# Kernel tuning notes

Hardware: AMD Instinct MI355X
Metric: run time of the kernel (lower is better)

Reference implementation:

```python
import jax, jax.numpy as jnp
import numpy as np

B, H, KVH, D = 64, 32, 8, 128     # batch, q heads, kv heads, head dim
BS, MB = 16, 128                  # paged-cache block size, max blocks per seq
NB = B * MB                       # total cache blocks (8192)
L = MB * BS                       # max kv length per sequence (2048)
SCALE = 0.08838834764831845       # 1/sqrt(head_dim)


def setup_inputs() -> dict:
    key = jax.random.key(0)
    ks = jax.random.split(key, 6)
    q = jax.random.normal(ks[0], (B, H * D), jnp.float32)
    k = jax.random.normal(ks[1], (B, KVH * D), jnp.float32)
    v = jax.random.normal(ks[2], (B, KVH * D), jnp.float32)
    k_cache = jax.random.normal(ks[3], (NB, BS, KVH, D), jnp.float32)
    v_cache = jax.random.normal(ks[4], (NB, BS, KVH, D), jnp.float32)
    # each sequence owns MB disjoint contiguous blocks
    block_tables = jnp.arange(B * MB, dtype=jnp.int32).reshape(B, MB)
    context_lens = jax.random.randint(ks[5], (B,), 0, L - 1, dtype=jnp.int32)
    return dict(q=q, k=k, v=v, k_cache=k_cache, v_cache=v_cache,
                block_tables=block_tables, context_lens=context_lens)


def reference(q, k, v, k_cache, v_cache, block_tables, context_lens):
    G = H // KVH  # GQA group size
    qh = q.reshape(B, KVH, G, D)
    kh = k.reshape(B, KVH, D)
    vh = v.reshape(B, KVH, D)
    # store new token's KV at its paged slot (position = context_len)
    slots = block_tables[jnp.arange(B), context_lens // BS] * BS + context_lens % BS
    kc = k_cache.reshape(NB * BS, KVH, D).at[slots].set(kh)
    vc = v_cache.reshape(NB * BS, KVH, D).at[slots].set(vh)
    # gather paged KV per sequence via block tables -> [B, L, KVH, D]
    keys = kc.reshape(NB, BS, KVH, D)[block_tables].reshape(B, L, KVH, D)
    vals = vc.reshape(NB, BS, KVH, D)[block_tables].reshape(B, L, KVH, D)
    # GQA attention: each kv head serves G query heads
    scores = jnp.einsum('bkgd,blkd->bkgl', qh, keys) * SCALE
    valid = jnp.arange(L)[None, :] <= context_lens[:, None]  # [B, L], inclusive of new token
    scores = jnp.where(valid[:, None, None, :], scores, jnp.float32(-jnp.inf))
    w = jax.nn.softmax(scores, axis=-1)
    out = jnp.einsum('bkgl,blkd->bkgd', w, vals)
    return out.reshape(B, H * D)
```

## Files before the change

### kernel.cpp

```cpp
#include <hip/hip_runtime.h>

#define BATCH 64
#define NHEADS 32
#define KVH 8
#define HDIM 128
#define GQA 4
#define BLKSZ 16
#define MAXBLK 128
#define MAXLEN 2048
#define SCALE 0.08838834764831845f

#define CHUNK 64
#define NPART (MAXLEN / CHUNK)
#define GSTRIDE 144
#define SLOT_BYTES 4096u
#define WS_FLOATS ((size_t)BATCH * NPART * KVH * GQA * GSTRIDE)

typedef unsigned int uint;
typedef float f32x4 __attribute__((ext_vector_type(4)));

struct KVBuf { float4 k0, k1, v0, v1; };

template<int CTRL>
__device__ __forceinline__ float dppAdd(float x) {
    int y = __builtin_amdgcn_update_dpp(0, __float_as_int(x), CTRL, 0xf, 0xf, false);
    return x + __int_as_float(y);
}

__device__ __forceinline__ float halfSum(float v, bool upper) {
    v = dppAdd<0x111>(v);
    v = dppAdd<0x112>(v);
    v = dppAdd<0x114>(v);
    v = dppAdd<0x118>(v);
    v = dppAdd<0x142>(v);
    const float lo = __int_as_float(__builtin_amdgcn_readlane(__float_as_int(v), 31));
    const float hi = __int_as_float(__builtin_amdgcn_readlane(__float_as_int(v), 63));
    return upper ? hi : lo;
}

__global__ __launch_bounds__(256, 4) void pa_partial(
    const float* __restrict__ q,
    const float* __restrict__ knew,
    const float* __restrict__ vnew,
    const float* __restrict__ k_cache,
    const float* __restrict__ v_cache,
    const int*   __restrict__ block_tables,
    const int*   __restrict__ context_lens,
    float* __restrict__ ws)
{
    const int bid  = blockIdx.x;
    const int part = bid & (NPART - 1);
    const int b    = bid >> 5;

    const int cl = context_lens[b];
    const int n  = cl + 1;
    const int p0 = part * CHUNK;
    if (p0 >= n) return;
    const int pend = min(p0 + CHUNK, n);

    const int tid  = threadIdx.x;
    const int kvh  = tid >> 5;
    const int lane = tid & 31;
    const bool upperHalf = (tid & 32) != 0;
    const uint laneByte = ((uint)kvh << 9) + ((uint)lane << 4);

    float4 qf[GQA];
    #pragma unroll
    for (int g = 0; g < GQA; ++g) {
        float4 t = *reinterpret_cast<const float4*>(
            &q[(size_t)b * (NHEADS * HDIM) + (size_t)(kvh * GQA + g) * HDIM + lane * 4]);
        t.x *= SCALE; t.y *= SCALE; t.z *= SCALE; t.w *= SCALE;
        qf[g] = t;
    }

    float  s[GQA];
    float4 acc[GQA];
    #pragma unroll
    for (int g = 0; g < GQA; ++g) {
        s[g] = 0.f;
        acc[g] = make_float4(0.f, 0.f, 0.f, 0.f);
    }

    const char* kc8 = reinterpret_cast<const char*>(k_cache);
    const char* vc8 = reinterpret_cast<const char*>(v_cache);

    if (p0 + CHUNK <= cl) {
        int blkv[4];
        #pragma unroll
        for (int c = 0; c < 4; ++c)
            blkv[c] = block_tables[b * MAXBLK + (p0 >> 4) + c];

        KVBuf bufA, bufB;

#define ISSUE(P, i)                                                              \
        {                                                                        \
            const uint u0 = ((uint)blkv[(2*(i)) >> 4] * BLKSZ + ((2*(i)) & 15)) * SLOT_BYTES + laneByte; \
            const uint u1 = ((uint)blkv[(2*(i)+1) >> 4] * BLKSZ + ((2*(i)+1) & 15)) * SLOT_BYTES + laneByte; \
            buf##P.k0 = *reinterpret_cast<const float4*>(kc8 + u0);              \
            buf##P.k1 = *reinterpret_cast<const float4*>(kc8 + u1);              \
            buf##P.v0 = *reinterpret_cast<const float4*>(vc8 + u0);              \
            buf##P.v1 = *reinterpret_cast<const float4*>(vc8 + u1);              \
        }

#define CONSUME(P)                                                               \
        {                                                                        \
            float sc0[GQA], sc1[GQA];                                            \
            _Pragma("unroll")                                                    \
            for (int g = 0; g < GQA; ++g) {                                      \
                sc0[g] = buf##P.k0.x * qf[g].x + buf##P.k0.y * qf[g].y           \
                       + buf##P.k0.z * qf[g].z + buf##P.k0.w * qf[g].w;          \
                sc1[g] = buf##P.k1.x * qf[g].x + buf##P.k1.y * qf[g].y           \
                       + buf##P.k1.z * qf[g].z + buf##P.k1.w * qf[g].w;          \
            }                                                                    \
            _Pragma("unroll")                                                    \
            for (int g = 0; g < GQA; ++g) {                                      \
                sc0[g] = halfSum(sc0[g], upperHalf);                             \
                sc1[g] = halfSum(sc1[g], upperHalf);                             \
            }                                                                    \
            _Pragma("unroll")                                                    \
            for (int g = 0; g < GQA; ++g) {                                      \
                const float e0 = __expf(sc0[g]);                                 \
                const float e1 = __expf(sc1[g]);                                 \
                s[g] += e0 + e1;                                                 \
                acc[g].x += e0 * buf##P.v0.x + e1 * buf##P.v1.x;                 \
                acc[g].y += e0 * buf##P.v0.y + e1 * buf##P.v1.y;                 \
                acc[g].z += e0 * buf##P.v0.z + e1 * buf##P.v1.z;                 \
                acc[g].w += e0 * buf##P.v0.w + e1 * buf##P.v1.w;                 \
            }                                                                    \
        }

        ISSUE(A, 0);
        #pragma unroll
        for (int i = 0; i < 31; ++i) {
            if (i & 1) { ISSUE(A, i + 1); CONSUME(B); }
            else       { ISSUE(B, i + 1); CONSUME(A); }
        }
        CONSUME(B);
#undef ISSUE
#undef CONSUME
    } else {
        const int* bt = &block_tables[b * MAXBLK];
        const float* knrow = &knew[((size_t)b * KVH + kvh) * HDIM + lane * 4];
        const float* vnrow = &vnew[((size_t)b * KVH + kvh) * HDIM + lane * 4];

        for (int t0 = p0; t0 < pend; t0 += 4) {
            bool valid[4];
            const float* kp[4];
            const float* vp[4];
            #pragma unroll
            for (int j = 0; j < 4; ++j) {
                const int l = t0 + j;
                valid[j] = (l < pend);
                if (!valid[j] || l == cl) {
                    kp[j] = knrow; vp[j] = vnrow;
                } else {
                    const int blk = bt[l >> 4];
                    const uint u  = ((uint)blk * BLKSZ + (l & 15)) * SLOT_BYTES + laneByte;
                    kp[j] = reinterpret_cast<const float*>(kc8 + u);
                    vp[j] = reinterpret_cast<const float*>(vc8 + u);
                }
            }

            float4 kf[4], vf[4];
            #pragma unroll
            for (int j = 0; j < 4; ++j) kf[j] = *reinterpret_cast<const float4*>(kp[j]);
            #pragma unroll
            for (int j = 0; j < 4; ++j) vf[j] = *reinterpret_cast<const float4*>(vp[j]);

            float sc[4][GQA];
            #pragma unroll
            for (int j = 0; j < 4; ++j)
                #pragma unroll
                for (int g = 0; g < GQA; ++g)
                    sc[j][g] = kf[j].x * qf[g].x + kf[j].y * qf[g].y
                             + kf[j].z * qf[g].z + kf[j].w * qf[g].w;

            #pragma unroll
            for (int off = 16; off > 0; off >>= 1)
                #pragma unroll
                for (int j = 0; j < 4; ++j)
                    #pragma unroll
                    for (int g = 0; g < GQA; ++g)
                        sc[j][g] += __shfl_xor(sc[j][g], off, 32);

            #pragma unroll
            for (int g = 0; g < GQA; ++g) {
                float p[4];
                #pragma unroll
                for (int j = 0; j < 4; ++j)
                    p[j] = valid[j] ? __expf(sc[j][g]) : 0.f;
                s[g] += (p[0] + p[1]) + (p[2] + p[3]);
                acc[g].x += p[0] * vf[0].x + p[1] * vf[1].x + p[2] * vf[2].x + p[3] * vf[3].x;
                acc[g].y += p[0] * vf[0].y + p[1] * vf[1].y + p[2] * vf[2].y + p[3] * vf[3].y;
                acc[g].z += p[0] * vf[0].z + p[1] * vf[1].z + p[2] * vf[2].z + p[3] * vf[3].z;
                acc[g].w += p[0] * vf[0].w + p[1] * vf[1].w + p[2] * vf[2].w + p[3] * vf[3].w;
            }
        }
    }

    float* rec = ws + ((size_t)(bid * KVH + kvh) * GQA) * GSTRIDE;
    #pragma unroll
    for (int g = 0; g < GQA; ++g)
        *reinterpret_cast<float4*>(rec + (size_t)g * GSTRIDE + lane * 4) = acc[g];
    if (lane == 0) {
        #pragma unroll
        for (int g = 0; g < GQA; ++g) rec[(size_t)g * GSTRIDE + 128] = s[g];
    }
}

__global__ __launch_bounds__(128) void pa_reduce(
    const float* __restrict__ ws,
    const int*   __restrict__ context_lens,
    float* __restrict__ out)
{
    const int bh   = blockIdx.x;
    const int b    = bh >> 3;
    const int kvh  = bh & 7;
    const int t    = threadIdx.x;
    const int g    = t >> 5;
    const int lane = t & 31;

    const int n    = context_lens[b] + 1;
    const int pcnt = (n + CHUNK - 1) / CHUNK;

    const float* base = ws + ((size_t)((b * NPART) * KVH + kvh) * GQA + g) * GSTRIDE;
    const size_t pstride = (size_t)KVH * GQA * GSTRIDE;

    f32x4 O0 = {0,0,0,0}, O1 = {0,0,0,0}, O2 = {0,0,0,0}, O3 = {0,0,0,0};
    float S0 = 0.f, S1 = 0.f, S2 = 0.f, S3 = 0.f;
    int p = 0;
    for (; p + 4 <= pcnt; p += 4) {
        const float* r0 = base + (p + 0) * pstride;
        const float* r1 = base + (p + 1) * pstride;
        const float* r2 = base + (p + 2) * pstride;
        const float* r3 = base + (p + 3) * pstride;
        O0 += *reinterpret_cast<const f32x4*>(r0 + lane * 4);
        O1 += *reinterpret_cast<const f32x4*>(r1 + lane * 4);
        O2 += *reinterpret_cast<const f32x4*>(r2 + lane * 4);
        O3 += *reinterpret_cast<const f32x4*>(r3 + lane * 4);
        S0 += r0[128]; S1 += r1[128]; S2 += r2[128]; S3 += r3[128];
    }
    for (; p < pcnt; ++p) {
        const float* r = base + p * pstride;
        O0 += *reinterpret_cast<const f32x4*>(r + lane * 4);
        S0 += r[128];
    }
    const f32x4 O = (O0 + O1) + (O2 + O3);
    const float S = (S0 + S1) + (S2 + S3);
    const float inv = 1.0f / S;

    float* op = &out[(size_t)b * (NHEADS * HDIM) + (size_t)(kvh * GQA + g) * HDIM + lane * 4];
    *reinterpret_cast<f32x4*>(op) = O * inv;
}

__global__ __launch_bounds__(256) void paged_attn_decode(
    const float* __restrict__ q,
    const float* __restrict__ knew,
    const float* __restrict__ vnew,
    const float* __restrict__ k_cache,
    const float* __restrict__ v_cache,
    const int*   __restrict__ block_tables,
    const int*   __restrict__ context_lens,
    float* __restrict__ out)
{
    const int bh   = blockIdx.x;
    const int b    = bh / KVH;
    const int kvh  = bh % KVH;
    const int tid  = threadIdx.x;
    const int hw   = tid >> 5;
    const int lane = tid & 31;

    const int cl = context_lens[b];
    const int n  = cl + 1;

    float4 qf[GQA];
    #pragma unroll
    for (int g = 0; g < GQA; ++g) {
        float4 t = *reinterpret_cast<const float4*>(
            &q[(size_t)b * (NHEADS * HDIM) + (size_t)(kvh * GQA + g) * HDIM + lane * 4]);
        t.x *= SCALE; t.y *= SCALE; t.z *= SCALE; t.w *= SCALE;
        qf[g] = t;
    }

    float  s[GQA];
    float4 acc[GQA];
    #pragma unroll
    for (int g = 0; g < GQA; ++g) { s[g] = 0.f; acc[g] = make_float4(0.f,0.f,0.f,0.f); }

    const int* bt = &block_tables[b * MAXBLK];

    for (int l = hw; l < n; l += 8) {
        const float4* krow;
        const float4* vrow;
        if (l == cl) {
            krow = reinterpret_cast<const float4*>(&knew[(size_t)(b * KVH + kvh) * HDIM]);
            vrow = reinterpret_cast<const float4*>(&vnew[(size_t)(b * KVH + kvh) * HDIM]);
        } else {
            const int    blk = bt[l >> 4];
            const size_t off = (((size_t)blk * BLKSZ + (l & 15)) * KVH + kvh) * HDIM;
            krow = reinterpret_cast<const float4*>(&k_cache[off]);
            vrow = reinterpret_cast<const float4*>(&v_cache[off]);
        }
        const float4 kf = krow[lane];
        const float4 vf = vrow[lane];

        float sc[GQA];
        #pragma unroll
        for (int g = 0; g < GQA; ++g)
            sc[g] = kf.x * qf[g].x + kf.y * qf[g].y + kf.z * qf[g].z + kf.w * qf[g].w;

        #pragma unroll
        for (int off = 16; off > 0; off >>= 1)
            #pragma unroll
            for (int g = 0; g < GQA; ++g)
                sc[g] += __shfl_xor(sc[g], off, 32);

        #pragma unroll
        for (int g = 0; g < GQA; ++g) {
            const float p = __expf(sc[g]);
            s[g] += p;
            acc[g].x += p * vf.x; acc[g].y += p * vf.y;
            acc[g].z += p * vf.z; acc[g].w += p * vf.w;
        }
    }

    __shared__ float lds_s[8][GQA];
    __shared__ float lds_acc[8][GQA][HDIM];

    #pragma unroll
    for (int g = 0; g < GQA; ++g)
        *reinterpret_cast<float4*>(&lds_acc[hw][g][lane * 4]) = acc[g];
    if (lane == 0) {
        #pragma unroll
        for (int g = 0; g < GQA; ++g) lds_s[hw][g] = s[g];
    }
    __syncthreads();

    for (int i = tid; i < GQA * HDIM; i += 256) {
        const int g = i >> 7;
        const int d = i & 127;
        float S = 0.f, O = 0.f;
        #pragma unroll
        for (int h = 0; h < 8; ++h) { S += lds_s[h][g]; O += lds_acc[h][g][d]; }
        out[(size_t)b * (NHEADS * HDIM) + (size_t)(kvh * GQA + g) * HDIM + d] = O / S;
    }
}

extern "C" void kernel_launch(void* const* d_in, const int* in_sizes, int n_in,
                              void* d_out, int out_size, void* d_ws, size_t ws_size,
                              hipStream_t stream) {
    const float* q      = (const float*)d_in[0];
    const float* k      = (const float*)d_in[1];
    const float* v      = (const float*)d_in[2];
    const float* kc     = (const float*)d_in[3];
    const float* vc     = (const float*)d_in[4];
    const int*   bt     = (const int*)d_in[5];
    const int*   clens  = (const int*)d_in[6];
    float*       out    = (float*)d_out;

    if (ws_size >= WS_FLOATS * sizeof(float)) {
        float* ws = (float*)d_ws;
        pa_partial<<<dim3(BATCH * NPART), dim3(256), 0, stream>>>(
            q, k, v, kc, vc, bt, clens, ws);
        pa_reduce<<<dim3(BATCH * KVH), dim3(128), 0, stream>>>(ws, clens, out);
    } else {
        paged_attn_decode<<<dim3(BATCH * KVH), dim3(256), 0, stream>>>(
            q, k, v, kc, vc, bt, clens, out);
    }
}
```

Before: 138.1 us.

## Compact split-K work items with a prefix-sum scan over context lengths

Adds a tiny scan kernel that prefix-sums the per-sequence chunk counts. The partial kernel then maps each block to a (batch, chunk) pair by binary search, so only real work items are packed at the front of the grid. This removes the scattered empty blocks that previously exited early and compacts the workspace records the reduce kernel reads. The cost is an extra kernel launch, a binary search per block, and a grid that still launches the maximum item count, with the unused tail exiting immediately.

After: 121.0 us. 12.4% less time.

```diff
diff --git a/kernel.cpp b/kernel.cpp
--- a/kernel.cpp
+++ b/kernel.cpp
@@ -11,10 +11,11 @@
 #define SCALE 0.08838834764831845f
 
 #define CHUNK 64
-#define NPART (MAXLEN / CHUNK)
+#define MAXITEMS 2048
 #define GSTRIDE 144
 #define SLOT_BYTES 4096u
-#define WS_FLOATS ((size_t)BATCH * NPART * KVH * GQA * GSTRIDE)
+#define WS_RECORDS ((size_t)MAXITEMS * KVH * GQA * GSTRIDE)
+#define WS_FLOATS  (WS_RECORDS + 80)
 
 typedef unsigned int uint;
 typedef float f32x4 __attribute__((ext_vector_type(4)));
@@ -38,6 +39,18 @@
     return upper ? hi : lo;
 }
 
+__global__ void pa_scan(const int* __restrict__ context_lens, uint* __restrict__ offs) {
+    const int t = threadIdx.x;
+    int cnt = (t < BATCH) ? (context_lens[t] + 1 + CHUNK - 1) / CHUNK : 0;
+    #pragma unroll
+    for (int o = 1; o < 64; o <<= 1) {
+        const int v = __shfl_up(cnt, o, 64);
+        if (t >= o) cnt += v;
+    }
+    offs[t + 1] = (uint)cnt;
+    if (t == 0) offs[0] = 0u;
+}
+
 __global__ __launch_bounds__(256, 4) void pa_partial(
     const float* __restrict__ q,
     const float* __restrict__ knew,
@@ -46,16 +59,23 @@
     const float* __restrict__ v_cache,
     const int*   __restrict__ block_tables,
     const int*   __restrict__ context_lens,
-    float* __restrict__ ws)
+    float* __restrict__ ws,
+    const uint*  __restrict__ offs)
 {
-    const int bid  = blockIdx.x;
-    const int part = bid & (NPART - 1);
-    const int b    = bid >> 5;
+    const uint item = blockIdx.x;
+    if (item >= offs[BATCH]) return;
+
+    int lo = 0, hi = BATCH;
+    while (lo + 1 < hi) {
+        const int mid = (lo + hi) >> 1;
+        if (item >= offs[mid]) lo = mid; else hi = mid;
+    }
+    const int b    = lo;
+    const int part = (int)(item - offs[b]);
 
     const int cl = context_lens[b];
     const int n  = cl + 1;
     const int p0 = part * CHUNK;
-    if (p0 >= n) return;
     const int pend = min(p0 + CHUNK, n);
 
     const int tid  = threadIdx.x;
@@ -198,7 +218,7 @@
         }
     }
 
-    float* rec = ws + ((size_t)(bid * KVH + kvh) * GQA) * GSTRIDE;
+    float* rec = ws + ((size_t)(item * KVH + kvh) * GQA) * GSTRIDE;
     #pragma unroll
     for (int g = 0; g < GQA; ++g)
         *reinterpret_cast<float4*>(rec + (size_t)g * GSTRIDE + lane * 4) = acc[g];
@@ -210,7 +230,7 @@
 
 __global__ __launch_bounds__(128) void pa_reduce(
     const float* __restrict__ ws,
-    const int*   __restrict__ context_lens,
+    const uint*  __restrict__ offs,
     float* __restrict__ out)
 {
     const int bh   = blockIdx.x;
@@ -220,10 +240,10 @@
     const int g    = t >> 5;
     const int lane = t & 31;
 
-    const int n    = context_lens[b] + 1;
-    const int pcnt = (n + CHUNK - 1) / CHUNK;
-
-    const float* base = ws + ((size_t)((b * NPART) * KVH + kvh) * GQA + g) * GSTRIDE;
+    const uint i0   = offs[b];
+    const int  pcnt = (int)(offs[b + 1] - i0);
+
+    const float* base = ws + ((size_t)(i0 * KVH + kvh) * GQA + g) * GSTRIDE;
     const size_t pstride = (size_t)KVH * GQA * GSTRIDE;
 
     f32x4 O0 = {0,0,0,0}, O1 = {0,0,0,0}, O2 = {0,0,0,0}, O3 = {0,0,0,0};
@@ -359,10 +379,12 @@
     float*       out    = (float*)d_out;
 
     if (ws_size >= WS_FLOATS * sizeof(float)) {
-        float* ws = (float*)d_ws;
-        pa_partial<<<dim3(BATCH * NPART), dim3(256), 0, stream>>>(
-            q, k, v, kc, vc, bt, clens, ws);
-        pa_reduce<<<dim3(BATCH * KVH), dim3(128), 0, stream>>>(ws, clens, out);
+        float* ws   = (float*)d_ws;
+        uint*  offs = (uint*)(ws + WS_RECORDS);
+        pa_scan<<<dim3(1), dim3(64), 0, stream>>>(clens, offs);
+        pa_partial<<<dim3(MAXITEMS), dim3(256), 0, stream>>>(
+            q, k, v, kc, vc, bt, clens, ws, offs);
+        pa_reduce<<<dim3(BATCH * KVH), dim3(128), 0, stream>>>(ws, offs, out);
     } else {
         paged_attn_decode<<<dim3(BATCH * KVH), dim3(256), 0, stream>>>(
             q, k, v, kc, vc, bt, clens, out);
```
